# Kernel optimization log

Hardware: AMD Instinct MI355X
Metric: run time of the kernel (lower is better)

The kernel has to match this reference:

```python
import jax, jax.numpy as jnp
import numpy as np

N = 50000      # nodes
E = 800000     # edges
CIN = 128
CH = 128
COUT = 64
EPS = 1e-5     # BatchNorm eps


def setup_inputs() -> dict:
    key = jax.random.key(0)
    ks = jax.random.split(key, 16)
    s = 0.1  # weight scale for numerical stability
    return {
        "x": jax.random.normal(ks[0], (N, CIN), jnp.float32),
        "edge_index": jax.random.randint(ks[1], (2, E), 0, N, jnp.int32),
        "edge_weights": jax.random.uniform(ks[2], (E,), jnp.float32),
        "w1": jax.random.normal(ks[3], (CIN, CH), jnp.float32) * s,
        "b1": jnp.zeros((CH,), jnp.float32),
        "bn1_g": jnp.ones((CH,), jnp.float32),
        "bn1_b": jnp.zeros((CH,), jnp.float32),
        "bn1_m": jax.random.normal(ks[4], (CH,), jnp.float32) * 0.1,
        "bn1_v": jax.random.uniform(ks[5], (CH,), jnp.float32) + 0.5,
        "conv_ws": jax.random.normal(ks[6], (2, CH, CH), jnp.float32) * s,
        "conv_bs": jnp.zeros((2, CH), jnp.float32),
        "bns_g": jnp.ones((2, CH), jnp.float32),
        "bns_b": jnp.zeros((2, CH), jnp.float32),
        "bns_m": jax.random.normal(ks[7], (2, CH), jnp.float32) * 0.1,
        "bns_v": jax.random.uniform(ks[8], (2, CH), jnp.float32) + 0.5,
        "lin1_w": jax.random.normal(ks[9], (CH, CH), jnp.float32) * s,
        "lin1_b": jnp.zeros((CH,), jnp.float32),
        "lin2_w": jax.random.normal(ks[10], (CH, COUT), jnp.float32) * s,
        "lin2_b": jnp.zeros((COUT,), jnp.float32),
    }


def _bn(h, g, b, m, v):
    # BatchNorm1d in eval mode: running statistics
    return (h - m) * jax.lax.rsqrt(v + EPS) * g + b


def _gcn(h, w, b, src, dst, norm, n):
    # GCNConv: out[dst] += norm_e * (h @ W)[src]  (self loops already in src/dst)
    h = h @ w
    msg = h[src] * norm[:, None]                 # [E+N, CH]
    return jax.ops.segment_sum(msg, dst, num_segments=n) + b


def reference(x, edge_index, edge_weights, w1, b1, bn1_g, bn1_b, bn1_m, bn1_v,
              conv_ws, conv_bs, bns_g, bns_b, bns_m, bns_v,
              lin1_w, lin1_b, lin2_w, lin2_b):
    n = x.shape[0]
    loop = jnp.arange(n, dtype=edge_index.dtype)
    src = jnp.concatenate([edge_index[0], loop])
    dst = jnp.concatenate([edge_index[1], loop])
    ew = jnp.concatenate([edge_weights, jnp.ones((n,), edge_weights.dtype)])
    # symmetric degree normalization (PyG gcn_norm)
    deg = jax.ops.segment_sum(ew, dst, num_segments=n)
    dis = jnp.where(deg > 0, jax.lax.rsqrt(deg), 0.0)
    norm = dis[src] * ew * dis[dst]

    lrelu = jax.nn.leaky_relu  # slope 0.01, matches F.leaky_relu default
    h = lrelu(_bn(_gcn(x, w1, b1, src, dst, norm, n), bn1_g, bn1_b, bn1_m, bn1_v))
    for i in range(conv_ws.shape[0]):
        h = lrelu(_bn(_gcn(h, conv_ws[i], conv_bs[i], src, dst, norm, n),
                      bns_g[i], bns_b[i], bns_m[i], bns_v[i]) + h)
    h = lrelu(h @ lin1_w + lin1_b)
    # dropout is identity in eval mode
    return h @ lin2_w + lin2_b
```

## Files before the change

kernel.cpp:

```cpp
#include <hip/hip_runtime.h>
#include <hip/hip_bf16.h>


constexpr int   NN    = 50000;
constexpr int   EE    = 800000;
constexpr int   CH    = 128;
constexpr int   SLOTS = 64;
constexpr int   NBUK  = 782;
constexpr int   RCAP  = 2048;
constexpr int   EPB   = 4096;
constexpr float EPS   = 1e-5f;

typedef __attribute__((ext_vector_type(8))) short bf16x8;
typedef __attribute__((ext_vector_type(4))) float f32x4;
typedef unsigned long long u64;
typedef unsigned short u16;

__device__ inline u16 f2bf_rne(float f) {
  unsigned u = __float_as_uint(f);
  unsigned r = u + 0x7fffu + ((u >> 16) & 1u);
  return (u16)(r >> 16);
}
__device__ inline float bf2f(unsigned h16) {
  return __uint_as_float(h16 << 16);
}


__global__ __launch_bounds__(256) void bin_kernel(const int* __restrict__ ei,
                                                  const float* __restrict__ ew,
                                                  unsigned* __restrict__ gcur,
                                                  u64* __restrict__ bins) {
  __shared__ unsigned cnt[NBUK];
  __shared__ unsigned base[NBUK];
  const int tid = threadIdx.x;
  for (int b = tid; b < NBUK; b += 256) cnt[b] = 0;
  __syncthreads();
  const int e0 = blockIdx.x * EPB;
  unsigned pk[16]; u16 bkt[16]; u16 rnk[16]; unsigned char dl[16];
  #pragma unroll
  for (int i = 0; i < 16; i++) {
    int e = e0 + i * 256 + tid;
    if (e < EE) {
      int s = ei[e], d = ei[EE + e];
      float w = ew[e];
      bkt[i] = (u16)(d >> 6);
      dl[i]  = (unsigned char)(d & 63);
      pk[i]  = ((unsigned)f2bf_rne(w) << 16) | (unsigned)s;
      rnk[i] = (u16)atomicAdd(&cnt[bkt[i]], 1u);
    } else bkt[i] = 0xffffu;
  }
  __syncthreads();
  for (int b = tid; b < NBUK; b += 256) {
    unsigned c = cnt[b];
    base[b] = c ? atomicAdd(&gcur[b * 16], c) : 0u;
  }
  __syncthreads();
  #pragma unroll
  for (int i = 0; i < 16; i++) {
    if (bkt[i] == 0xffffu) continue;
    unsigned pos = base[bkt[i]] + rnk[i];
    if (pos < RCAP)
      bins[(size_t)bkt[i] * RCAP + pos] = ((u64)dl[i] << 32) | pk[i];
  }
}


__global__ __launch_bounds__(256) void scatter_kernel(const unsigned* __restrict__ gcur,
                                                      const u64* __restrict__ bins,
                                                      unsigned* __restrict__ ell,
                                                      float* __restrict__ dis) {
  __shared__ unsigned rank[64];
  __shared__ float    wsum[64];
  const int b   = blockIdx.x;
  const int tid = threadIdx.x;
  if (tid < 64) { rank[tid] = 1u; wsum[tid] = 0.f; }
  __syncthreads();
  unsigned cnt = gcur[b * 16];
  if (cnt > RCAP) cnt = RCAP;
  const u64* src = bins + (size_t)b * RCAP;
  for (unsigned i = tid; i < cnt; i += 256) {
    u64 v = src[i];
    unsigned pk = (unsigned)v;
    unsigned dl = (unsigned)(v >> 32);
    unsigned r = atomicAdd(&rank[dl], 1u);
    if (r < SLOTS)
      ell[((size_t)(b * 64 + dl)) * SLOTS + r] = pk;
    atomicAdd(&wsum[dl], bf2f(pk >> 16));
  }
  __syncthreads();
  if (tid < 64) {
    int node = b * 64 + tid;
    if (node < NN) {
      unsigned c = rank[tid];
      if (c > SLOTS) c = SLOTS;
      ell[(size_t)node * SLOTS] = c;
      dis[node] = rsqrtf(1.0f + wsum[tid]);
    }
  }
}

constexpr int NB_WZ = (73728 + 384 + 255) / 256;

__global__ void wswz_kernel(
    const float* __restrict__ w1, const float* __restrict__ bn1_g, const float* __restrict__ bn1_v,
    const float* __restrict__ conv_ws, const float* __restrict__ bns_g, const float* __restrict__ bns_v,
    const float* __restrict__ lin1_w, const float* __restrict__ lin2_w,
    const float* __restrict__ b1, const float* __restrict__ bn1_b, const float* __restrict__ bn1_m,
    const float* __restrict__ conv_bs, const float* __restrict__ bns_b, const float* __restrict__ bns_m,
    u16* __restrict__ w1h, u16* __restrict__ w1l,
    u16* __restrict__ c0h, u16* __restrict__ c0l,
    u16* __restrict__ c1h, u16* __restrict__ c1l,
    u16* __restrict__ l1h, u16* __restrict__ l1l,
    u16* __restrict__ l2h, u16* __restrict__ l2l,
    float* __restrict__ beff)
{
  int idx = blockIdx.x * 256 + threadIdx.x;
  if (idx >= 73728) {
    int r = idx - 73728;
    if (r >= 384) return;
    int l = r >> 7, c = r & 127;
    float bc, gg, bb, mm, vv;
    if (l == 0) { bc = b1[c]; gg = bn1_g[c]; bb = bn1_b[c]; mm = bn1_m[c]; vv = bn1_v[c]; }
    else {
      int o = (l - 1) * 128 + c;
      bc = conv_bs[o]; gg = bns_g[o]; bb = bns_b[o]; mm = bns_m[o]; vv = bns_v[o];
    }
    beff[r] = (bc - mm) * gg * rsqrtf(vv + EPS) + bb;
    return;
  }
  const float* W; const float* g = nullptr; const float* v = nullptr;
  u16 *hi, *lo; int CO = 128; int local;
  if      (idx < 16384) { W = w1;              g = bn1_g;     v = bn1_v;     hi = w1h; lo = w1l; local = idx; }
  else if (idx < 32768) { W = conv_ws;         g = bns_g;     v = bns_v;     hi = c0h; lo = c0l; local = idx - 16384; }
  else if (idx < 49152) { W = conv_ws + 16384; g = bns_g+128; v = bns_v+128; hi = c1h; lo = c1l; local = idx - 32768; }
  else if (idx < 65536) { W = lin1_w;                                        hi = l1h; lo = l1l; local = idx - 49152; }
  else                  { W = lin2_w;                                        hi = l2h; lo = l2l; local = idx - 65536; CO = 64; }
  int k = local / CO, n = local % CO;
  float w = W[local];
  if (g) w *= g[n] * rsqrtf(v[n] + EPS);
  int NCT = CO / 16;
  int kchunk = k >> 5, kin = k & 31, quad = kin >> 3, j = kin & 7;
  int ct = n >> 4, l = (quad << 4) | (n & 15);
  size_t pos = ((size_t)(kchunk * NCT + ct) * 64 + l) * 8 + j;
  u16 h = f2bf_rne(w);
  hi[pos] = h;
  lo[pos] = f2bf_rne(w - bf2f(h));
}

__global__ __launch_bounds__(256) void gemm1_kernel(
    const float* __restrict__ Ain,
    const u16* __restrict__ Whi, const u16* __restrict__ Wlo,
    const float* __restrict__ dis, u16* __restrict__ Cout)
{
  __shared__ float lds[64][CH + 4];
  const int tid  = threadIdx.x;
  const int wave = tid >> 6;
  const int lane = tid & 63;
  const int quad = lane >> 4;
  const int mrow = lane & 15;
  const int row0 = blockIdx.x * 64;

  int arow = row0 + wave * 16 + mrow;
  if (arow >= NN) arow = NN - 1;

  bf16x8 ahi[4], alo[4];
  const float* Ar = Ain + (size_t)arow * CH;
  #pragma unroll
  for (int c = 0; c < 4; c++) {
    int off = c * 32 + quad * 8;
    float4 f0 = *(const float4*)(Ar + off);
    float4 f1 = *(const float4*)(Ar + off + 4);
    float f[8] = {f0.x, f0.y, f0.z, f0.w, f1.x, f1.y, f1.z, f1.w};
    #pragma unroll
    for (int j = 0; j < 8; j++) {
      u16 h = f2bf_rne(f[j]);
      ahi[c][j] = (short)h;
      alo[c][j] = (short)f2bf_rne(f[j] - bf2f(h));
    }
  }

  f32x4 acc[8];
  #pragma unroll
  for (int t = 0; t < 8; t++) acc[t] = (f32x4){0.f, 0.f, 0.f, 0.f};
  #pragma unroll
  for (int c = 0; c < 4; c++) {
    #pragma unroll
    for (int t = 0; t < 8; t++) {
      size_t base = ((size_t)(c * 8 + t) * 64 + lane) * 8;
      bf16x8 bh = *(const bf16x8*)(Whi + base);
      bf16x8 bl = *(const bf16x8*)(Wlo + base);
      acc[t] = __builtin_amdgcn_mfma_f32_16x16x32_bf16(ahi[c], bh, acc[t], 0, 0, 0);
      acc[t] = __builtin_amdgcn_mfma_f32_16x16x32_bf16(alo[c], bh, acc[t], 0, 0, 0);
      acc[t] = __builtin_amdgcn_mfma_f32_16x16x32_bf16(ahi[c], bl, acc[t], 0, 0, 0);
    }
  }

  #pragma unroll
  for (int t = 0; t < 8; t++)
    #pragma unroll
    for (int r = 0; r < 4; r++)
      lds[wave * 16 + quad * 4 + r][t * 16 + mrow] = acc[t][r];
  __syncthreads();

  #pragma unroll
  for (int i = tid; i < 64 * CH / 4; i += 256) {
    int row = (i * 4) / CH;
    int col = (i * 4) % CH;
    int grow = row0 + row;
    if (grow >= NN) continue;
    float rs = dis[grow];
    const float* lp = &lds[row][col];
    u16* cp = (u16*)Cout + (size_t)grow * CH + col;
    unsigned p0 = ((unsigned)f2bf_rne(lp[1] * rs) << 16) | f2bf_rne(lp[0] * rs);
    unsigned p1 = ((unsigned)f2bf_rne(lp[3] * rs) << 16) | f2bf_rne(lp[2] * rs);
    *(uint2*)cp = make_uint2(p0, p1);
  }
}

template<bool RES>
__global__ __launch_bounds__(256) void fuse_kernel(
    const u16* __restrict__ hwin,
    const unsigned* __restrict__ ell, const float* __restrict__ dis,
    const float* __restrict__ beff, const u16* __restrict__ res,
    const u16* __restrict__ Whi, const u16* __restrict__ Wlo,
    u16* __restrict__ hout, u16* __restrict__ hwout)
{
  __shared__ float lds[64][CH + 4];
  const int tid  = threadIdx.x;
  const int wave = tid >> 6;
  const int lane = tid & 63;
  const int sub  = lane & 15;
  const int grp  = lane >> 4;
  const int row0 = blockIdx.x * 64;

  for (int r = 0; r < 16; r++) {
    int node = row0 + wave * 16 + r;
    int nd = node < NN ? node : NN - 1;
    unsigned myword = ell[(size_t)nd * SLOTS + lane];
    int cnt = __shfl((int)myword, 0);
    if (cnt > SLOTS) cnt = SLOTS;
    float a[8] = {0.f, 0.f, 0.f, 0.f, 0.f, 0.f, 0.f, 0.f};
    for (int j = 0; j < cnt; j += 8) {
      int j0 = j + grp, j1 = j + 4 + grp;
      unsigned e0 = (unsigned)__shfl((int)myword, j0 & 63);
      unsigned e1 = (unsigned)__shfl((int)myword, j1 & 63);
      float    w0 = (j0 == 0) ? 1.0f : bf2f(e0 >> 16);
      unsigned s0 = (j0 == 0) ? (unsigned)nd : (e0 & 0xffffu);
      float    w1 = bf2f(e1 >> 16);
      unsigned s1 = e1 & 0xffffu;
      if (j0 >= cnt) { w0 = 0.f; s0 = (unsigned)nd; }
      if (j1 >= cnt) { w1 = 0.f; s1 = (unsigned)nd; }
      uint4 h0 = *(const uint4*)(hwin + (size_t)s0 * CH + sub * 8);
      uint4 h1 = *(const uint4*)(hwin + (size_t)s1 * CH + sub * 8);
      a[0] = fmaf(w0, bf2f(h0.x & 0xffffu), a[0]); a[1] = fmaf(w0, bf2f(h0.x >> 16), a[1]);
      a[2] = fmaf(w0, bf2f(h0.y & 0xffffu), a[2]); a[3] = fmaf(w0, bf2f(h0.y >> 16), a[3]);
      a[4] = fmaf(w0, bf2f(h0.z & 0xffffu), a[4]); a[5] = fmaf(w0, bf2f(h0.z >> 16), a[5]);
      a[6] = fmaf(w0, bf2f(h0.w & 0xffffu), a[6]); a[7] = fmaf(w0, bf2f(h0.w >> 16), a[7]);
      a[0] = fmaf(w1, bf2f(h1.x & 0xffffu), a[0]); a[1] = fmaf(w1, bf2f(h1.x >> 16), a[1]);
      a[2] = fmaf(w1, bf2f(h1.y & 0xffffu), a[2]); a[3] = fmaf(w1, bf2f(h1.y >> 16), a[3]);
      a[4] = fmaf(w1, bf2f(h1.z & 0xffffu), a[4]); a[5] = fmaf(w1, bf2f(h1.z >> 16), a[5]);
      a[6] = fmaf(w1, bf2f(h1.w & 0xffffu), a[6]); a[7] = fmaf(w1, bf2f(h1.w >> 16), a[7]);
    }
    #pragma unroll
    for (int k = 0; k < 8; k++) {
      a[k] += __shfl_xor(a[k], 16);
      a[k] += __shfl_xor(a[k], 32);
    }
    if (grp == 0) {
      float disd = dis[nd];
      int c = sub * 8;
      float4 be0 = *(const float4*)(beff + c);
      float4 be1 = *(const float4*)(beff + c + 4);
      float y[8];
      y[0] = a[0] * disd + be0.x; y[1] = a[1] * disd + be0.y;
      y[2] = a[2] * disd + be0.z; y[3] = a[3] * disd + be0.w;
      y[4] = a[4] * disd + be1.x; y[5] = a[5] * disd + be1.y;
      y[6] = a[6] * disd + be1.z; y[7] = a[7] * disd + be1.w;
      if constexpr (RES) {
        uint4 rr = *(const uint4*)(res + (size_t)nd * CH + c);
        y[0] += bf2f(rr.x & 0xffffu); y[1] += bf2f(rr.x >> 16);
        y[2] += bf2f(rr.y & 0xffffu); y[3] += bf2f(rr.y >> 16);
        y[4] += bf2f(rr.z & 0xffffu); y[5] += bf2f(rr.z >> 16);
        y[6] += bf2f(rr.w & 0xffffu); y[7] += bf2f(rr.w >> 16);
      }
      #pragma unroll
      for (int k = 0; k < 8; k++) y[k] = y[k] > 0.f ? y[k] : 0.01f * y[k];
      uint4 o;
      o.x = ((unsigned)f2bf_rne(y[1]) << 16) | f2bf_rne(y[0]);
      o.y = ((unsigned)f2bf_rne(y[3]) << 16) | f2bf_rne(y[2]);
      o.z = ((unsigned)f2bf_rne(y[5]) << 16) | f2bf_rne(y[4]);
      o.w = ((unsigned)f2bf_rne(y[7]) << 16) | f2bf_rne(y[6]);
      if (node < NN) *(uint4*)(hout + (size_t)node * CH + c) = o;
      float* lp = &lds[wave * 16 + r][c];
      lp[0] = bf2f(o.x & 0xffffu); lp[1] = bf2f(o.x >> 16);
      lp[2] = bf2f(o.y & 0xffffu); lp[3] = bf2f(o.y >> 16);
      lp[4] = bf2f(o.z & 0xffffu); lp[5] = bf2f(o.z >> 16);
      lp[6] = bf2f(o.w & 0xffffu); lp[7] = bf2f(o.w >> 16);
    }
  }
  __syncthreads();

  bf16x8 af[4];
  {
    const float* hr = lds[wave * 16 + sub];
    #pragma unroll
    for (int c = 0; c < 4; c++) {
      const float* p = hr + c * 32 + grp * 8;
      #pragma unroll
      for (int j = 0; j < 8; j++) af[c][j] = (short)f2bf_rne(p[j]);
    }
  }
  __syncthreads();

  f32x4 acc[8];
  #pragma unroll
  for (int t = 0; t < 8; t++) acc[t] = (f32x4){0.f, 0.f, 0.f, 0.f};
  #pragma unroll
  for (int c = 0; c < 4; c++) {
    #pragma unroll
    for (int t = 0; t < 8; t++) {
      size_t base = ((size_t)(c * 8 + t) * 64 + lane) * 8;
      bf16x8 bh = *(const bf16x8*)(Whi + base);
      bf16x8 bl = *(const bf16x8*)(Wlo + base);
      acc[t] = __builtin_amdgcn_mfma_f32_16x16x32_bf16(af[c], bh, acc[t], 0, 0, 0);
      acc[t] = __builtin_amdgcn_mfma_f32_16x16x32_bf16(af[c], bl, acc[t], 0, 0, 0);
    }
  }

  #pragma unroll
  for (int t = 0; t < 8; t++)
    #pragma unroll
    for (int r = 0; r < 4; r++)
      lds[wave * 16 + grp * 4 + r][t * 16 + sub] = acc[t][r];
  __syncthreads();

  #pragma unroll
  for (int i = tid; i < 64 * CH / 4; i += 256) {
    int row = (i * 4) / CH;
    int col = (i * 4) % CH;
    int grow = row0 + row;
    if (grow >= NN) continue;
    float rs = dis[grow];
    const float* lp = &lds[row][col];
    u16* cp = hwout + (size_t)grow * CH + col;
    unsigned p0 = ((unsigned)f2bf_rne(lp[1] * rs) << 16) | f2bf_rne(lp[0] * rs);
    unsigned p1 = ((unsigned)f2bf_rne(lp[3] * rs) << 16) | f2bf_rne(lp[2] * rs);
    *(uint2*)cp = make_uint2(p0, p1);
  }
}

__global__ __launch_bounds__(256) void fuse_last_kernel(
    const u16* __restrict__ hwin,
    const unsigned* __restrict__ ell, const float* __restrict__ dis,
    const float* __restrict__ beff, const u16* __restrict__ res,
    const u16* __restrict__ l1h, const u16* __restrict__ l1l,
    const float* __restrict__ b1,
    const u16* __restrict__ l2h, const u16* __restrict__ l2l,
    const float* __restrict__ b2, float* __restrict__ out)
{
  __shared__ float lds[64][CH + 4];
  const int tid  = threadIdx.x;
  const int wave = tid >> 6;
  const int lane = tid & 63;
  const int sub  = lane & 15;
  const int grp  = lane >> 4;
  const int row0 = blockIdx.x * 64;

  for (int r = 0; r < 16; r++) {
    int node = row0 + wave * 16 + r;
    int nd = node < NN ? node : NN - 1;
    unsigned myword = ell[(size_t)nd * SLOTS + lane];
    int cnt = __shfl((int)myword, 0);
    if (cnt > SLOTS) cnt = SLOTS;
    float a[8] = {0.f, 0.f, 0.f, 0.f, 0.f, 0.f, 0.f, 0.f};
    for (int j = 0; j < cnt; j += 8) {
      int j0 = j + grp, j1 = j + 4 + grp;
      unsigned e0 = (unsigned)__shfl((int)myword, j0 & 63);
      unsigned e1 = (unsigned)__shfl((int)myword, j1 & 63);
      float    w0 = (j0 == 0) ? 1.0f : bf2f(e0 >> 16);
      unsigned s0 = (j0 == 0) ? (unsigned)nd : (e0 & 0xffffu);
      float    w1 = bf2f(e1 >> 16);
      unsigned s1 = e1 & 0xffffu;
      if (j0 >= cnt) { w0 = 0.f; s0 = (unsigned)nd; }
      if (j1 >= cnt) { w1 = 0.f; s1 = (unsigned)nd; }
      uint4 h0 = *(const uint4*)(hwin + (size_t)s0 * CH + sub * 8);
      uint4 h1 = *(const uint4*)(hwin + (size_t)s1 * CH + sub * 8);
      a[0] = fmaf(w0, bf2f(h0.x & 0xffffu), a[0]); a[1] = fmaf(w0, bf2f(h0.x >> 16), a[1]);
      a[2] = fmaf(w0, bf2f(h0.y & 0xffffu), a[2]); a[3] = fmaf(w0, bf2f(h0.y >> 16), a[3]);
      a[4] = fmaf(w0, bf2f(h0.z & 0xffffu), a[4]); a[5] = fmaf(w0, bf2f(h0.z >> 16), a[5]);
      a[6] = fmaf(w0, bf2f(h0.w & 0xffffu), a[6]); a[7] = fmaf(w0, bf2f(h0.w >> 16), a[7]);
      a[0] = fmaf(w1, bf2f(h1.x & 0xffffu), a[0]); a[1] = fmaf(w1, bf2f(h1.x >> 16), a[1]);
      a[2] = fmaf(w1, bf2f(h1.y & 0xffffu), a[2]); a[3] = fmaf(w1, bf2f(h1.y >> 16), a[3]);
      a[4] = fmaf(w1, bf2f(h1.z & 0xffffu), a[4]); a[5] = fmaf(w1, bf2f(h1.z >> 16), a[5]);
      a[6] = fmaf(w1, bf2f(h1.w & 0xffffu), a[6]); a[7] = fmaf(w1, bf2f(h1.w >> 16), a[7]);
    }
    #pragma unroll
    for (int k = 0; k < 8; k++) {
      a[k] += __shfl_xor(a[k], 16);
      a[k] += __shfl_xor(a[k], 32);
    }
    if (grp == 0) {
      float disd = dis[nd];
      int c = sub * 8;
      float4 be0 = *(const float4*)(beff + c);
      float4 be1 = *(const float4*)(beff + c + 4);
      float y[8];
      y[0] = a[0] * disd + be0.x; y[1] = a[1] * disd + be0.y;
      y[2] = a[2] * disd + be0.z; y[3] = a[3] * disd + be0.w;
      y[4] = a[4] * disd + be1.x; y[5] = a[5] * disd + be1.y;
      y[6] = a[6] * disd + be1.z; y[7] = a[7] * disd + be1.w;
      uint4 rr = *(const uint4*)(res + (size_t)nd * CH + c);
      y[0] += bf2f(rr.x & 0xffffu); y[1] += bf2f(rr.x >> 16);
      y[2] += bf2f(rr.y & 0xffffu); y[3] += bf2f(rr.y >> 16);
      y[4] += bf2f(rr.z & 0xffffu); y[5] += bf2f(rr.z >> 16);
      y[6] += bf2f(rr.w & 0xffffu); y[7] += bf2f(rr.w >> 16);
      float* lp = &lds[wave * 16 + r][c];
      #pragma unroll
      for (int k = 0; k < 8; k++) {
        float x = y[k] > 0.f ? y[k] : 0.01f * y[k];
        lp[k] = bf2f(f2bf_rne(x));
      }
    }
  }
  __syncthreads();

  bf16x8 af[4];
  {
    const float* hr = lds[wave * 16 + sub];
    #pragma unroll
    for (int c = 0; c < 4; c++) {
      const float* p = hr + c * 32 + grp * 8;
      #pragma unroll
      for (int j = 0; j < 8; j++) af[c][j] = (short)f2bf_rne(p[j]);
    }
  }
  __syncthreads();

  f32x4 acc[8];
  #pragma unroll
  for (int t = 0; t < 8; t++) acc[t] = (f32x4){0.f, 0.f, 0.f, 0.f};
  #pragma unroll
  for (int c = 0; c < 4; c++) {
    #pragma unroll
    for (int t = 0; t < 8; t++) {
      size_t base = ((size_t)(c * 8 + t) * 64 + lane) * 8;
      bf16x8 bh = *(const bf16x8*)(l1h + base);
      bf16x8 bl = *(const bf16x8*)(l1l + base);
      acc[t] = __builtin_amdgcn_mfma_f32_16x16x32_bf16(af[c], bh, acc[t], 0, 0, 0);
      acc[t] = __builtin_amdgcn_mfma_f32_16x16x32_bf16(af[c], bl, acc[t], 0, 0, 0);
    }
  }
  #pragma unroll
  for (int t = 0; t < 8; t++) {
    float bb = b1[t * 16 + sub];
    #pragma unroll
    for (int r = 0; r < 4; r++) {
      float x = acc[t][r] + bb;
      x = x > 0.f ? x : 0.01f * x;
      lds[wave * 16 + grp * 4 + r][t * 16 + sub] = x;
    }
  }
  __syncthreads();

  f32x4 acc2[4];
  #pragma unroll
  for (int t = 0; t < 4; t++) acc2[t] = (f32x4){0.f, 0.f, 0.f, 0.f};
  const int lrow = wave * 16 + sub;
  #pragma unroll
  for (int c = 0; c < 4; c++) {
    bf16x8 ahi, alo;
    const float* lp = &lds[lrow][c * 32 + grp * 8];
    float4 f0 = *(const float4*)lp;
    float4 f1 = *(const float4*)(lp + 4);
    float f[8] = {f0.x, f0.y, f0.z, f0.w, f1.x, f1.y, f1.z, f1.w};
    #pragma unroll
    for (int j = 0; j < 8; j++) {
      u16 h = f2bf_rne(f[j]);
      ahi[j] = (short)h;
      alo[j] = (short)f2bf_rne(f[j] - bf2f(h));
    }
    #pragma unroll
    for (int t = 0; t < 4; t++) {
      size_t base = ((size_t)(c * 4 + t) * 64 + lane) * 8;
      bf16x8 bh = *(const bf16x8*)(l2h + base);
      bf16x8 bl = *(const bf16x8*)(l2l + base);
      acc2[t] = __builtin_amdgcn_mfma_f32_16x16x32_bf16(ahi, bh, acc2[t], 0, 0, 0);
      acc2[t] = __builtin_amdgcn_mfma_f32_16x16x32_bf16(alo, bh, acc2[t], 0, 0, 0);
      acc2[t] = __builtin_amdgcn_mfma_f32_16x16x32_bf16(ahi, bl, acc2[t], 0, 0, 0);
    }
  }
  #pragma unroll
  for (int t = 0; t < 4; t++) {
    float bb = b2[t * 16 + sub];
    #pragma unroll
    for (int r = 0; r < 4; r++) {
      int grow = row0 + wave * 16 + grp * 4 + r;
      if (grow < NN)
        out[(size_t)grow * 64 + t * 16 + sub] = acc2[t][r] + bb;
    }
  }
}


extern "C" void kernel_launch(void* const* d_in, const int* in_sizes, int n_in,
                              void* d_out, int out_size, void* d_ws, size_t ws_size,
                              hipStream_t stream) {
  const float* x       = (const float*)d_in[0];
  const int*   ei      = (const int*)  d_in[1];
  const float* ew      = (const float*)d_in[2];
  const float* w1      = (const float*)d_in[3];
  const float* b1      = (const float*)d_in[4];
  const float* bn1_g   = (const float*)d_in[5];
  const float* bn1_b   = (const float*)d_in[6];
  const float* bn1_m   = (const float*)d_in[7];
  const float* bn1_v   = (const float*)d_in[8];
  const float* conv_ws = (const float*)d_in[9];
  const float* conv_bs = (const float*)d_in[10];
  const float* bns_g   = (const float*)d_in[11];
  const float* bns_b   = (const float*)d_in[12];
  const float* bns_m   = (const float*)d_in[13];
  const float* bns_v   = (const float*)d_in[14];
  const float* lin1_w  = (const float*)d_in[15];
  const float* lin1_b  = (const float*)d_in[16];
  const float* lin2_w  = (const float*)d_in[17];
  const float* lin2_b  = (const float*)d_in[18];
  float* out = (float*)d_out;

  size_t off = 0;
  auto alloc = [&](size_t elems) -> void* {
    void* p = (char*)d_ws + off * 4;
    off += (elems + 3) & ~(size_t)3;
    return p;
  };
  unsigned* gcur = (unsigned*)alloc(NBUK * 16);
  u64*      bins = (u64*)     alloc((size_t)NBUK * RCAP * 2);
  unsigned* ell  = (unsigned*)alloc((size_t)NN * SLOTS);
  float*    dis  = (float*)   alloc(NN);
  float*    beff = (float*)   alloc(3 * CH);
  u16*      hwa  = (u16*)     alloc((size_t)NN * CH / 2);
  u16*      hwb  = (u16*)     alloc((size_t)NN * CH / 2);
  u16*      h1   = (u16*)     alloc((size_t)NN * CH / 2);
  u16*      h2   = (u16*)     alloc((size_t)NN * CH / 2);
  u16* w1h = (u16*)alloc(CH * CH / 2); u16* w1l = (u16*)alloc(CH * CH / 2);
  u16* c0h = (u16*)alloc(CH * CH / 2); u16* c0l = (u16*)alloc(CH * CH / 2);
  u16* c1h = (u16*)alloc(CH * CH / 2); u16* c1l = (u16*)alloc(CH * CH / 2);
  u16* l1h = (u16*)alloc(CH * CH / 2); u16* l1l = (u16*)alloc(CH * CH / 2);
  u16* l2h = (u16*)alloc(CH * 64 / 2); u16* l2l = (u16*)alloc(CH * 64 / 2);

  const int nb_bin  = (EE + EPB - 1) / EPB;
  const int nb_gemm = (NN + 63) / 64;
  dim3 B(256);

  hipMemsetAsync(gcur, 0, NBUK * 16 * sizeof(unsigned), stream);
  bin_kernel    <<<nb_bin, B, 0, stream>>>(ei, ew, gcur, bins);
  scatter_kernel<<<NBUK,   B, 0, stream>>>(gcur, bins, ell, dis);

  wswz_kernel<<<NB_WZ, B, 0, stream>>>(w1, bn1_g, bn1_v, conv_ws, bns_g, bns_v,
      lin1_w, lin2_w, b1, bn1_b, bn1_m, conv_bs, bns_b, bns_m,
      w1h, w1l, c0h, c0l, c1h, c1l, l1h, l1l, l2h, l2l, beff);

  gemm1_kernel<<<nb_gemm, B, 0, stream>>>(x, w1h, w1l, dis, hwa);

  fuse_kernel<false><<<nb_gemm, B, 0, stream>>>(hwa, ell, dis, beff, nullptr,
      c0h, c0l, h1, hwb);

  fuse_kernel<true><<<nb_gemm, B, 0, stream>>>(hwb, ell, dis, beff + CH, h1,
      c1h, c1l, h2, hwa);

  fuse_last_kernel<<<nb_gemm, B, 0, stream>>>(hwa, ell, dis, beff + 2 * CH, h2,
      l1h, l1l, lin1_b, l2h, l2l, lin2_b, out);
}
```

Before: 315.2 us.

## Store bf16 tiles in LDS, drop block barriers, deepen gather unroll

The fused aggregation+GEMM kernels now keep per-wave tiles as packed bf16 in a smaller shared array instead of fp32. This removes the fp32 round trip and the block-wide __syncthreads, since each wave only reads its own 16 rows. The neighbour gather loop now issues four independent row loads per iteration instead of two, to keep more memory requests in flight. Launch bounds now ask for higher occupancy, and the hwout epilogue writes straight from MFMA accumulators with scattered 2-byte stores. That store pattern is less coalesced, and the occupancy request may force register spills.

```diff
diff --git a/kernel.cpp b/kernel.cpp
--- a/kernel.cpp
+++ b/kernel.cpp
@@ -218,14 +218,14 @@
 }
 
 template<bool RES>
-__global__ __launch_bounds__(256) void fuse_kernel(
+__global__ __launch_bounds__(256, 5) void fuse_kernel(
     const u16* __restrict__ hwin,
     const unsigned* __restrict__ ell, const float* __restrict__ dis,
     const float* __restrict__ beff, const u16* __restrict__ res,
     const u16* __restrict__ Whi, const u16* __restrict__ Wlo,
     u16* __restrict__ hout, u16* __restrict__ hwout)
 {
-  __shared__ float lds[64][CH + 4];
+  __shared__ unsigned hs[64][68];
   const int tid  = threadIdx.x;
   const int wave = tid >> 6;
   const int lane = tid & 63;
@@ -240,26 +240,29 @@
     int cnt = __shfl((int)myword, 0);
     if (cnt > SLOTS) cnt = SLOTS;
     float a[8] = {0.f, 0.f, 0.f, 0.f, 0.f, 0.f, 0.f, 0.f};
-    for (int j = 0; j < cnt; j += 8) {
-      int j0 = j + grp, j1 = j + 4 + grp;
-      unsigned e0 = (unsigned)__shfl((int)myword, j0 & 63);
-      unsigned e1 = (unsigned)__shfl((int)myword, j1 & 63);
-      float    w0 = (j0 == 0) ? 1.0f : bf2f(e0 >> 16);
-      unsigned s0 = (j0 == 0) ? (unsigned)nd : (e0 & 0xffffu);
-      float    w1 = bf2f(e1 >> 16);
-      unsigned s1 = e1 & 0xffffu;
-      if (j0 >= cnt) { w0 = 0.f; s0 = (unsigned)nd; }
-      if (j1 >= cnt) { w1 = 0.f; s1 = (unsigned)nd; }
-      uint4 h0 = *(const uint4*)(hwin + (size_t)s0 * CH + sub * 8);
-      uint4 h1 = *(const uint4*)(hwin + (size_t)s1 * CH + sub * 8);
-      a[0] = fmaf(w0, bf2f(h0.x & 0xffffu), a[0]); a[1] = fmaf(w0, bf2f(h0.x >> 16), a[1]);
-      a[2] = fmaf(w0, bf2f(h0.y & 0xffffu), a[2]); a[3] = fmaf(w0, bf2f(h0.y >> 16), a[3]);
-      a[4] = fmaf(w0, bf2f(h0.z & 0xffffu), a[4]); a[5] = fmaf(w0, bf2f(h0.z >> 16), a[5]);
-      a[6] = fmaf(w0, bf2f(h0.w & 0xffffu), a[6]); a[7] = fmaf(w0, bf2f(h0.w >> 16), a[7]);
-      a[0] = fmaf(w1, bf2f(h1.x & 0xffffu), a[0]); a[1] = fmaf(w1, bf2f(h1.x >> 16), a[1]);
-      a[2] = fmaf(w1, bf2f(h1.y & 0xffffu), a[2]); a[3] = fmaf(w1, bf2f(h1.y >> 16), a[3]);
-      a[4] = fmaf(w1, bf2f(h1.z & 0xffffu), a[4]); a[5] = fmaf(w1, bf2f(h1.z >> 16), a[5]);
-      a[6] = fmaf(w1, bf2f(h1.w & 0xffffu), a[6]); a[7] = fmaf(w1, bf2f(h1.w >> 16), a[7]);
+    for (int j = 0; j < cnt; j += 16) {
+      unsigned sidx[4]; float wv[4];
+      #pragma unroll
+      for (int q = 0; q < 4; q++) {
+        int jj = j + q * 4 + grp;
+        unsigned e = (unsigned)__shfl((int)myword, jj & 63);
+        float    w = (jj == 0) ? 1.0f : bf2f(e >> 16);
+        unsigned s = (jj == 0) ? (unsigned)nd : (e & 0xffffu);
+        if (jj >= cnt) { w = 0.f; s = (unsigned)nd; }
+        sidx[q] = s; wv[q] = w;
+      }
+      uint4 h[4];
+      #pragma unroll
+      for (int q = 0; q < 4; q++)
+        h[q] = *(const uint4*)(hwin + (size_t)sidx[q] * CH + sub * 8);
+      #pragma unroll
+      for (int q = 0; q < 4; q++) {
+        float w = wv[q];
+        a[0] = fmaf(w, bf2f(h[q].x & 0xffffu), a[0]); a[1] = fmaf(w, bf2f(h[q].x >> 16), a[1]);
+        a[2] = fmaf(w, bf2f(h[q].y & 0xffffu), a[2]); a[3] = fmaf(w, bf2f(h[q].y >> 16), a[3]);
+        a[4] = fmaf(w, bf2f(h[q].z & 0xffffu), a[4]); a[5] = fmaf(w, bf2f(h[q].z >> 16), a[5]);
+        a[6] = fmaf(w, bf2f(h[q].w & 0xffffu), a[6]); a[7] = fmaf(w, bf2f(h[q].w >> 16), a[7]);
+      }
     }
     #pragma unroll
     for (int k = 0; k < 8; k++) {
@@ -291,26 +294,14 @@
       o.z = ((unsigned)f2bf_rne(y[5]) << 16) | f2bf_rne(y[4]);
       o.w = ((unsigned)f2bf_rne(y[7]) << 16) | f2bf_rne(y[6]);
       if (node < NN) *(uint4*)(hout + (size_t)node * CH + c) = o;
-      float* lp = &lds[wave * 16 + r][c];
-      lp[0] = bf2f(o.x & 0xffffu); lp[1] = bf2f(o.x >> 16);
-      lp[2] = bf2f(o.y & 0xffffu); lp[3] = bf2f(o.y >> 16);
-      lp[4] = bf2f(o.z & 0xffffu); lp[5] = bf2f(o.z >> 16);
-      lp[6] = bf2f(o.w & 0xffffu); lp[7] = bf2f(o.w >> 16);
-    }
-  }
-  __syncthreads();
+      *(uint4*)&hs[wave * 16 + r][sub * 4] = o;
+    }
+  }
 
   bf16x8 af[4];
-  {
-    const float* hr = lds[wave * 16 + sub];
-    #pragma unroll
-    for (int c = 0; c < 4; c++) {
-      const float* p = hr + c * 32 + grp * 8;
-      #pragma unroll
-      for (int j = 0; j < 8; j++) af[c][j] = (short)f2bf_rne(p[j]);
-    }
-  }
-  __syncthreads();
+  #pragma unroll
+  for (int c = 0; c < 4; c++)
+    af[c] = *(const bf16x8*)&hs[wave * 16 + sub][c * 16 + grp * 4];
 
   f32x4 acc[8];
   #pragma unroll
@@ -328,28 +319,17 @@
   }
 
   #pragma unroll
-  for (int t = 0; t < 8; t++)
-    #pragma unroll
-    for (int r = 0; r < 4; r++)
-      lds[wave * 16 + grp * 4 + r][t * 16 + sub] = acc[t][r];
-  __syncthreads();
-
-  #pragma unroll
-  for (int i = tid; i < 64 * CH / 4; i += 256) {
-    int row = (i * 4) / CH;
-    int col = (i * 4) % CH;
-    int grow = row0 + row;
+  for (int r = 0; r < 4; r++) {
+    int grow = row0 + wave * 16 + grp * 4 + r;
     if (grow >= NN) continue;
     float rs = dis[grow];
-    const float* lp = &lds[row][col];
-    u16* cp = hwout + (size_t)grow * CH + col;
-    unsigned p0 = ((unsigned)f2bf_rne(lp[1] * rs) << 16) | f2bf_rne(lp[0] * rs);
-    unsigned p1 = ((unsigned)f2bf_rne(lp[3] * rs) << 16) | f2bf_rne(lp[2] * rs);
-    *(uint2*)cp = make_uint2(p0, p1);
-  }
-}
-
-__global__ __launch_bounds__(256) void fuse_last_kernel(
+    #pragma unroll
+    for (int t = 0; t < 8; t++)
+      hwout[(size_t)grow * CH + t * 16 + sub] = f2bf_rne(acc[t][r] * rs);
+  }
+}
+
+__global__ __launch_bounds__(256, 4) void fuse_last_kernel(
     const u16* __restrict__ hwin,
     const unsigned* __restrict__ ell, const float* __restrict__ dis,
     const float* __restrict__ beff, const u16* __restrict__ res,
@@ -358,7 +338,8 @@
     const u16* __restrict__ l2h, const u16* __restrict__ l2l,
     const float* __restrict__ b2, float* __restrict__ out)
 {
-  __shared__ float lds[64][CH + 4];
+  __shared__ unsigned smem[64 * 132];
+  float* fs = (float*)smem;
   const int tid  = threadIdx.x;
   const int wave = tid >> 6;
   const int lane = tid & 63;
@@ -373,26 +354,29 @@
     int cnt = __shfl((int)myword, 0);
     if (cnt > SLOTS) cnt = SLOTS;
     float a[8] = {0.f, 0.f, 0.f, 0.f, 0.f, 0.f, 0.f, 0.f};
-    for (int j = 0; j < cnt; j += 8) {
-      int j0 = j + grp, j1 = j + 4 + grp;
-      unsigned e0 = (unsigned)__shfl((int)myword, j0 & 63);
-      unsigned e1 = (unsigned)__shfl((int)myword, j1 & 63);
-      float    w0 = (j0 == 0) ? 1.0f : bf2f(e0 >> 16);
-      unsigned s0 = (j0 == 0) ? (unsigned)nd : (e0 & 0xffffu);
-      float    w1 = bf2f(e1 >> 16);
-      unsigned s1 = e1 & 0xffffu;
-      if (j0 >= cnt) { w0 = 0.f; s0 = (unsigned)nd; }
-      if (j1 >= cnt) { w1 = 0.f; s1 = (unsigned)nd; }
-      uint4 h0 = *(const uint4*)(hwin + (size_t)s0 * CH + sub * 8);
-      uint4 h1 = *(const uint4*)(hwin + (size_t)s1 * CH + sub * 8);
-      a[0] = fmaf(w0, bf2f(h0.x & 0xffffu), a[0]); a[1] = fmaf(w0, bf2f(h0.x >> 16), a[1]);
-      a[2] = fmaf(w0, bf2f(h0.y & 0xffffu), a[2]); a[3] = fmaf(w0, bf2f(h0.y >> 16), a[3]);
-      a[4] = fmaf(w0, bf2f(h0.z & 0xffffu), a[4]); a[5] = fmaf(w0, bf2f(h0.z >> 16), a[5]);
-      a[6] = fmaf(w0, bf2f(h0.w & 0xffffu), a[6]); a[7] = fmaf(w0, bf2f(h0.w >> 16), a[7]);
-      a[0] = fmaf(w1, bf2f(h1.x & 0xffffu), a[0]); a[1] = fmaf(w1, bf2f(h1.x >> 16), a[1]);
-      a[2] = fmaf(w1, bf2f(h1.y & 0xffffu), a[2]); a[3] = fmaf(w1, bf2f(h1.y >> 16), a[3]);
-      a[4] = fmaf(w1, bf2f(h1.z & 0xffffu), a[4]); a[5] = fmaf(w1, bf2f(h1.z >> 16), a[5]);
-      a[6] = fmaf(w1, bf2f(h1.w & 0xffffu), a[6]); a[7] = fmaf(w1, bf2f(h1.w >> 16), a[7]);
+    for (int j = 0; j < cnt; j += 16) {
+      unsigned sidx[4]; float wv[4];
+      #pragma unroll
+      for (int q = 0; q < 4; q++) {
+        int jj = j + q * 4 + grp;
+        unsigned e = (unsigned)__shfl((int)myword, jj & 63);
+        float    w = (jj == 0) ? 1.0f : bf2f(e >> 16);
+        unsigned s = (jj == 0) ? (unsigned)nd : (e & 0xffffu);
+        if (jj >= cnt) { w = 0.f; s = (unsigned)nd; }
+        sidx[q] = s; wv[q] = w;
+      }
+      uint4 h[4];
+      #pragma unroll
+      for (int q = 0; q < 4; q++)
+        h[q] = *(const uint4*)(hwin + (size_t)sidx[q] * CH + sub * 8);
+      #pragma unroll
+      for (int q = 0; q < 4; q++) {
+        float w = wv[q];
+        a[0] = fmaf(w, bf2f(h[q].x & 0xffffu), a[0]); a[1] = fmaf(w, bf2f(h[q].x >> 16), a[1]);
+        a[2] = fmaf(w, bf2f(h[q].y & 0xffffu), a[2]); a[3] = fmaf(w, bf2f(h[q].y >> 16), a[3]);
+        a[4] = fmaf(w, bf2f(h[q].z & 0xffffu), a[4]); a[5] = fmaf(w, bf2f(h[q].z >> 16), a[5]);
+        a[6] = fmaf(w, bf2f(h[q].w & 0xffffu), a[6]); a[7] = fmaf(w, bf2f(h[q].w >> 16), a[7]);
+      }
     }
     #pragma unroll
     for (int k = 0; k < 8; k++) {
@@ -414,26 +398,21 @@
       y[2] += bf2f(rr.y & 0xffffu); y[3] += bf2f(rr.y >> 16);
       y[4] += bf2f(rr.z & 0xffffu); y[5] += bf2f(rr.z >> 16);
       y[6] += bf2f(rr.w & 0xffffu); y[7] += bf2f(rr.w >> 16);
-      float* lp = &lds[wave * 16 + r][c];
-      #pragma unroll
-      for (int k = 0; k < 8; k++) {
-        float x = y[k] > 0.f ? y[k] : 0.01f * y[k];
-        lp[k] = bf2f(f2bf_rne(x));
-      }
-    }
-  }
-  __syncthreads();
+      #pragma unroll
+      for (int k = 0; k < 8; k++) y[k] = y[k] > 0.f ? y[k] : 0.01f * y[k];
+      uint4 o;
+      o.x = ((unsigned)f2bf_rne(y[1]) << 16) | f2bf_rne(y[0]);
+      o.y = ((unsigned)f2bf_rne(y[3]) << 16) | f2bf_rne(y[2]);
+      o.z = ((unsigned)f2bf_rne(y[5]) << 16) | f2bf_rne(y[4]);
+      o.w = ((unsigned)f2bf_rne(y[7]) << 16) | f2bf_rne(y[6]);
+      *(uint4*)&smem[(wave * 16 + r) * 68 + sub * 4] = o;
+    }
+  }
 
   bf16x8 af[4];
-  {
-    const float* hr = lds[wave * 16 + sub];
-    #pragma unroll
-    for (int c = 0; c < 4; c++) {
-      const float* p = hr + c * 32 + grp * 8;
-      #pragma unroll
-      for (int j = 0; j < 8; j++) af[c][j] = (short)f2bf_rne(p[j]);
-    }
-  }
+  #pragma unroll
+  for (int c = 0; c < 4; c++)
+    af[c] = *(const bf16x8*)&smem[(wave * 16 + sub) * 68 + c * 16 + grp * 4];
   __syncthreads();
 
   f32x4 acc[8];
@@ -457,19 +436,17 @@
     for (int r = 0; r < 4; r++) {
       float x = acc[t][r] + bb;
       x = x > 0.f ? x : 0.01f * x;
-      lds[wave * 16 + grp * 4 + r][t * 16 + sub] = x;
-    }
-  }
-  __syncthreads();
+      fs[(wave * 16 + grp * 4 + r) * 132 + t * 16 + sub] = x;
+    }
+  }
 
   f32x4 acc2[4];
   #pragma unroll
   for (int t = 0; t < 4; t++) acc2[t] = (f32x4){0.f, 0.f, 0.f, 0.f};
-  const int lrow = wave * 16 + sub;
   #pragma unroll
   for (int c = 0; c < 4; c++) {
     bf16x8 ahi, alo;
-    const float* lp = &lds[lrow][c * 32 + grp * 8];
+    const float* lp = &fs[(wave * 16 + sub) * 132 + c * 32 + grp * 8];
     float4 f0 = *(const float4*)lp;
     float4 f1 = *(const float4*)(lp + 4);
     float f[8] = {f0.x, f0.y, f0.z, f0.w, f1.x, f1.y, f1.z, f1.w};
```

Result: no change. 314.2 us (-0.3%).
